# Kernel tuning notes

Hardware: AMD Instinct MI355X
Metric: run time of the kernel (lower is better)

## Reference

```python
import jax, jax.numpy as jnp
import numpy as np

TAU = 1.2  # relaxed-categorical temperature (forward default)


def setup_inputs() -> dict:
    key = jax.random.key(0)
    ks = jax.random.split(key, 8)
    B, F, V, E, H, T = 1024, 2048, 4096, 256, 1024, 32
    n = lambda k, shape: jax.random.normal(k, shape, jnp.float32) * 0.1
    return {
        "t": jax.random.normal(ks[0], (B, F), jnp.float32),
        "embedding": n(ks[1], (V, E)),
        "aff_w": n(ks[2], (H, F)),
        "aff_b": jnp.zeros((H,), jnp.float32),
        "w_ih": n(ks[3], (4 * H, E)),
        "w_hh": n(ks[4], (4 * H, H)),
        "b_ih": jnp.zeros((4 * H,), jnp.float32),
        # PyTorch init: forget-gate bias (second quarter) set to 1
        "b_hh": jnp.zeros((4 * H,), jnp.float32).at[H:2 * H].set(1.0),
        "lp_w": n(ks[5], (V, H)),
        "lp_b": jnp.zeros((V,), jnp.float32),
        "start_token_idx": 1,
        "max_sentence_length": T,
    }


def reference(t, embedding, aff_w, aff_b, w_ih, w_hh, b_ih, b_hh, lp_w, lp_b,
              start_token_idx, max_sentence_length):
    B = t.shape[0]
    H = aff_w.shape[0]
    V = embedding.shape[0]

    h0 = t @ aff_w.T + aff_b                      # [B, H]
    c0 = jnp.zeros((B, H), t.dtype)
    tok0 = jax.nn.one_hot(jnp.full((B,), start_token_idx), V, dtype=t.dtype)

    # Gumbel noise for RelaxedOneHotCategorical rsample, one slab per step
    gumbel = jax.random.gumbel(jax.random.key(42), (max_sentence_length, B, V), t.dtype)

    def step(carry, g):
        h, c, tok = carry
        emb = tok @ embedding                     # [B, E] (one-hot/relaxed matmul)
        gates = emb @ w_ih.T + b_ih + h @ w_hh.T + b_hh  # [B, 4H]
        i, f, gg, o = jnp.split(gates, 4, axis=-1)        # PyTorch gate order i,f,g,o
        c = jax.nn.sigmoid(f) * c + jax.nn.sigmoid(i) * jnp.tanh(gg)
        h = jax.nn.sigmoid(o) * jnp.tanh(c)
        # softmax probs -> relaxed sample: softmax((log p + G)/tau)
        logp = jax.nn.log_softmax(h @ lp_w.T + lp_b, axis=-1)  # [B, V]
        y = jax.nn.softmax((logp + g) / TAU, axis=-1)
        hard = jax.nn.one_hot(jnp.argmax(y, axis=-1), V, dtype=y.dtype)
        tok = jax.lax.stop_gradient(hard - y) + y  # straight-through
        return (h, c, tok), tok

    _, toks = jax.lax.scan(step, (h0, c0, tok0), gumbel)  # toks: [T, B, V]
    message = jnp.concatenate([tok0[None], toks], axis=0)  # [T+1, B, V]
    return jnp.transpose(message, (1, 0, 2))               # [B, T+1, V]
```

## Files before the change

kernel.cpp:

```cpp
#include <hip/hip_runtime.h>
#include <math.h>


typedef _Float16 f16;
typedef f16 f16x8 __attribute__((ext_vector_type(8)));
typedef float f32x4 __attribute__((ext_vector_type(4)));

#define F16_MIN_NORM 6.104e-5f

__device__ __forceinline__ void split_f16(float v, f16& h, f16& l) {
  f16 h0 = (fabsf(v) < F16_MIN_NORM) ? (f16)0.0f : (f16)v;
  float r = (v - (float)h0) * 4096.0f;
  h = h0; l = (f16)r;
}

__device__ __forceinline__ float sigm(float x) { return 1.0f / (1.0f + expf(-x)); }

#define GLOAD_LDS16(gsrc, ldst)                                               \
  __builtin_amdgcn_global_load_lds(                                           \
      (const __attribute__((address_space(1))) unsigned int*)(const void*)(gsrc), \
      (__attribute__((address_space(3))) unsigned int*)(void*)(ldst), 16, 0, 0)


__device__ __forceinline__ unsigned tf_rotl(unsigned x, int r) {
  return (x << r) | (x >> (32 - r));
}

__device__ inline float gumbel_at(unsigned idx) {
  const unsigned ks0 = 0u;
  const unsigned ks1 = 42u;
  const unsigned ks2 = 0x1BD11BDAu ^ ks0 ^ ks1;
  unsigned x0 = 0u + ks0;
  unsigned x1 = idx + ks1;
#define TFR(rot) { x0 += x1; x1 = tf_rotl(x1, rot); x1 ^= x0; }
  TFR(13) TFR(15) TFR(26) TFR(6)
  x0 += ks1; x1 += ks2 + 1u;
  TFR(17) TFR(29) TFR(16) TFR(24)
  x0 += ks2; x1 += ks0 + 2u;
  TFR(13) TFR(15) TFR(26) TFR(6)
  x0 += ks0; x1 += ks1 + 3u;
  TFR(17) TFR(29) TFR(16) TFR(24)
  x0 += ks1; x1 += ks2 + 4u;
  TFR(13) TFR(15) TFR(26) TFR(6)
  x0 += ks2; x1 += ks0 + 5u;
#undef TFR
  const unsigned bits = x0 ^ x1;
  const float f = __uint_as_float((bits >> 9) | 0x3F800000u) - 1.0f;
  const float tiny = 1.17549435082228751e-38f;
  const float u = fmaxf(tiny, f * (1.0f - tiny) + tiny);
  return -logf(-logf(u));
}


__global__ void init_kernel(float* __restrict__ out, const int* __restrict__ startp,
                            int* __restrict__ tok, int Tp1, int V) {
  const int b = blockIdx.x;
  const int start = *startp;
  if (threadIdx.x == 0) tok[b] = start;
  float* orow = out + (size_t)b * Tp1 * V;
  const int tq = start >> 2;
  for (int v4 = threadIdx.x; v4 < V / 4; v4 += blockDim.x) {
    float4 v = make_float4(0.f, 0.f, 0.f, 0.f);
    if (v4 == tq) ((float*)&v)[start & 3] = 1.0f;
    ((float4*)orow)[v4] = v;
  }
}

__global__ void pack_gates_kernel(const float* __restrict__ wih,
                                  const float* __restrict__ whh,
                                  f16* __restrict__ w0, f16* __restrict__ w1,
                                  int E, int H, int K) {
  const int k = blockIdx.x * blockDim.x + threadIdx.x;
  const int p = blockIdx.y;
  if (k >= K) return;
  const int n = ((p >> 4) & 3) * H + ((p >> 6) << 4) + (p & 15);
  const float v = (k < E) ? wih[(size_t)n * E + k] : whh[(size_t)n * H + (k - E)];
  f16 h, l; split_f16(v, h, l);
  w0[(size_t)p * K + k] = h;
  w1[(size_t)p * K + k] = l;
}

__global__ void pack_bias_kernel(const float* __restrict__ bih,
                                 const float* __restrict__ bhh,
                                 float* __restrict__ bi, float* __restrict__ bh, int H) {
  const int p = blockIdx.x * blockDim.x + threadIdx.x;
  const int n = ((p >> 4) & 3) * H + ((p >> 6) << 4) + (p & 15);
  bi[p] = bih[n];
  bh[p] = bhh[n];
}

__global__ void split_kernel(const float* __restrict__ in,
                             f16* __restrict__ o0, f16* __restrict__ o1, int n) {
  const int i = blockIdx.x * blockDim.x + threadIdx.x;
  if (i < n) { f16 h, l; split_f16(in[i], h, l); o0[i] = h; o1[i] = l; }
}


__device__ __forceinline__ void stage_chunk(
    int chunk, int srow, int scol,
    const f16* __restrict__ a0s, const f16* __restrict__ a1s, int lda, int ka, int bm,
    const f16* __restrict__ b0s, const f16* __restrict__ b1s, int ldb, int kb, int bn,
    f16 (*ldsA0)[32], f16 (*ldsA1)[32], f16 (*ldsB0)[32], f16 (*ldsB1)[32])
{
  if (chunk < 8) {
    GLOAD_LDS16(a0s + (size_t)(bm + chunk * 16 + srow) * lda + ka + scol,
                &ldsA0[chunk * 16][0]);
  } else if (chunk < 16) {
    const int s = chunk - 8;
    GLOAD_LDS16(a1s + (size_t)(bm + s * 16 + srow) * lda + ka + scol,
                &ldsA1[s * 16][0]);
  } else if (chunk < 24) {
    const int s = chunk - 16;
    GLOAD_LDS16(b0s + (size_t)(bn + s * 16 + srow) * ldb + kb + scol,
                &ldsB0[s * 16][0]);
  } else {
    const int s = chunk - 24;
    GLOAD_LDS16(b1s + (size_t)(bn + s * 16 + srow) * ldb + kb + scol,
                &ldsB1[s * 16][0]);
  }
}

#define MFMA_DECLS                                                            \
  const int tid  = threadIdx.x;                                               \
  const int lane = tid & 63;                                                  \
  const int wid  = tid >> 6;                                                  \
  const int bm   = blockIdx.y * 128;                                          \
  const int bn   = blockIdx.x * 128;                                          \
  const int wm   = (wid & 3) * 32;                                            \
  const int wn   = (wid >> 2) * 64;                                           \
  const int fr   = lane & 15;                                                 \
  const int fk   = (((lane >> 4) ^ ((lane >> 1) & 3)) * 8);                   \
  const int srow = lane >> 2;                                                 \
  const int scol = (((lane & 3) ^ ((lane >> 3) & 3)) * 8);                    \
  f32x4 acc0[2][4], acc1[2][4];                                               \
  _Pragma("unroll") for (int i = 0; i < 2; ++i)                               \
  _Pragma("unroll") for (int j = 0; j < 4; ++j) {                             \
    acc0[i][j] = (f32x4)0.0f; acc1[i][j] = (f32x4)0.0f; }

#define MFMA_LDS_DECL                                                         \
  __shared__ f16 ldsA0[4][128][32], ldsA1[4][128][32],                        \
                 ldsB0[4][128][32], ldsB1[4][128][32];

#define MFMA_STAGE_TO(buf, a0s, a1s, lda, ka, b0s, b1s, ldb, kb)              \
  { _Pragma("unroll") for (int c = 0; c < 4; ++c)                             \
      stage_chunk(wid * 4 + c, srow, scol, (a0s), (a1s), (lda), (ka), bm,     \
                  (b0s), (b1s), (ldb), (kb), bn,                              \
                  ldsA0[(buf)], ldsA1[(buf)], ldsB0[(buf)], ldsB1[(buf)]); }

#define MFMA_COMPUTE_FROM(buf)                                                \
  {                                                                           \
    f16x8 a0[2], a1[2], b0[4], b1[4];                                         \
    _Pragma("unroll") for (int i = 0; i < 2; ++i) {                           \
      a0[i] = *(const f16x8*)&ldsA0[(buf)][wm + i * 16 + fr][fk];             \
      a1[i] = *(const f16x8*)&ldsA1[(buf)][wm + i * 16 + fr][fk];             \
    }                                                                         \
    _Pragma("unroll") for (int j = 0; j < 4; ++j) {                           \
      b0[j] = *(const f16x8*)&ldsB0[(buf)][wn + j * 16 + fr][fk];             \
      b1[j] = *(const f16x8*)&ldsB1[(buf)][wn + j * 16 + fr][fk];             \
    }                                                                         \
    _Pragma("unroll") for (int i = 0; i < 2; ++i)                             \
    _Pragma("unroll") for (int j = 0; j < 4; ++j) {                           \
      acc0[i][j] = __builtin_amdgcn_mfma_f32_16x16x32_f16(a0[i], b0[j], acc0[i][j], 0, 0, 0); \
      acc1[i][j] = __builtin_amdgcn_mfma_f32_16x16x32_f16(a0[i], b1[j], acc1[i][j], 0, 0, 0); \
      acc1[i][j] = __builtin_amdgcn_mfma_f32_16x16x32_f16(a1[i], b0[j], acc1[i][j], 0, 0, 0); \
    }                                                                         \
  }

#define PIPE(NT)                                                              \
  STAGE_T(0, 0)                                                               \
  STAGE_T(1, 1)                                                               \
  STAGE_T(2, 2)                                                               \
  for (int t = 0; t < (NT); ++t) {                                            \
    asm volatile("" ::: "memory");                                            \
    if (t + 3 < (NT)) { STAGE_T(((t + 3) & 3), (t + 3)) }                     \
    const int rem = (NT) - 1 - t;                                             \
    if (rem >= 3)      asm volatile("s_waitcnt vmcnt(12)" ::: "memory");      \
    else if (rem == 2) asm volatile("s_waitcnt vmcnt(8)" ::: "memory");       \
    else if (rem == 1) asm volatile("s_waitcnt vmcnt(4)" ::: "memory");       \
    else               asm volatile("s_waitcnt vmcnt(0)" ::: "memory");       \
    __builtin_amdgcn_s_barrier();                                             \
    asm volatile("" ::: "memory");                                            \
    __builtin_amdgcn_s_setprio(1);                                            \
    MFMA_COMPUTE_FROM((t & 3))                                                \
    __builtin_amdgcn_s_setprio(0);                                            \
    asm volatile("" ::: "memory");                                            \
    __builtin_amdgcn_s_barrier();                                             \
  }

__global__ __launch_bounds__(512, 2) void h0_kernel(
    const f16* __restrict__ t0, const f16* __restrict__ t1, int F,
    const f16* __restrict__ aw0, const f16* __restrict__ aw1,
    const float* __restrict__ affb,
    f16* __restrict__ h0p, f16* __restrict__ h1p, int H,
    float* __restrict__ czero)
{
  MFMA_LDS_DECL
  MFMA_DECLS
  const int NT = F / 32;
#define STAGE_T(buf, t) MFMA_STAGE_TO(buf, t0, t1, F, (t) * 32, aw0, aw1, F, (t) * 32)
  PIPE(NT)
#undef STAGE_T
  const int q4 = (lane >> 4) * 4;
  const float s12 = 1.0f / 4096.0f;
  const int cn0 = bn + wn;
#pragma unroll
  for (int j = 0; j < 4; ++j) {
    const int col = cn0 + j * 16 + fr;
    const float bb = affb[col];
#pragma unroll
    for (int i = 0; i < 2; ++i) {
#pragma unroll
      for (int r = 0; r < 4; ++r) {
        const int row = bm + wm + i * 16 + q4 + r;
        const float v = (acc0[i][j][r] + acc1[i][j][r] * s12) + bb;
        f16 hh, hl; split_f16(v, hh, hl);
        const size_t off = (size_t)row * H + col;
        h0p[off] = hh; h1p[off] = hl;
        czero[off] = 0.0f;
      }
    }
  }
}

__global__ __launch_bounds__(512, 2) void gih_kernel(
    const f16* __restrict__ e0, const f16* __restrict__ e1, int E,
    const f16* __restrict__ w0, const f16* __restrict__ w1, int K,
    const float* __restrict__ bi, const float* __restrict__ bh,
    float* __restrict__ gih, int NP)
{
  MFMA_LDS_DECL
  MFMA_DECLS
  const int NT = E / 32;
#define STAGE_T(buf, t) MFMA_STAGE_TO(buf, e0, e1, E, (t) * 32, w0, w1, K, (t) * 32)
  PIPE(NT)
#undef STAGE_T
  const int q4 = (lane >> 4) * 4;
  const float s12 = 1.0f / 4096.0f;
  const int cn0 = bn + wn;
#pragma unroll
  for (int j = 0; j < 4; ++j) {
    const int col = cn0 + j * 16 + fr;
    const float bb = bi[col] + bh[col];
#pragma unroll
    for (int i = 0; i < 2; ++i)
#pragma unroll
      for (int r = 0; r < 4; ++r) {
        const int row = bm + wm + i * 16 + q4 + r;
        gih[(size_t)row * NP + col] = (acc0[i][j][r] + acc1[i][j][r] * s12) + bb;
      }
  }
}

__global__ __launch_bounds__(512, 2) void gates_kernel(
    const f16* __restrict__ hin0, const f16* __restrict__ hin1, int H,
    const f16* __restrict__ w0, const f16* __restrict__ w1, int K, int E,
    const float* __restrict__ gih, int NP, const int* __restrict__ tok,
    float* __restrict__ cbuf,
    f16* __restrict__ hout0, f16* __restrict__ hout1)
{
  MFMA_LDS_DECL
  MFMA_DECLS
  const int NT = H / 32;
#define STAGE_T(buf, t) MFMA_STAGE_TO(buf, hin0, hin1, H, (t) * 32, w0, w1, K, E + (t) * 32)
  PIPE(NT)
#undef STAGE_T
  const int q4 = (lane >> 4) * 4;
  const float s12 = 1.0f / 4096.0f;
  const int cn0 = bn + wn;
  const int nunit = (cn0 >> 2) + fr;
#pragma unroll
  for (int i = 0; i < 2; ++i) {
#pragma unroll
    for (int r = 0; r < 4; ++r) {
      const int row = bm + wm + i * 16 + q4 + r;
      const float* gr = gih + (size_t)tok[row] * NP + cn0 + fr;
      float gv[4];
#pragma unroll
      for (int j = 0; j < 4; ++j)
        gv[j] = (acc0[i][j][r] + acc1[i][j][r] * s12) + gr[j * 16];
      const size_t off = (size_t)row * H + nunit;
      const float c = cbuf[off];
      const float cn = __fadd_rn(__fmul_rn(sigm(gv[1]), c),
                                 __fmul_rn(sigm(gv[0]), tanhf(gv[2])));
      const float hn = __fmul_rn(sigm(gv[3]), tanhf(cn));
      cbuf[off] = cn;
      f16 hh, hl; split_f16(hn, hh, hl);
      hout0[off] = hh; hout1[off] = hl;
    }
  }
}

__global__ __launch_bounds__(512, 2) void logits_kernel(
    const f16* __restrict__ h0p, const f16* __restrict__ h1p, int H,
    const f16* __restrict__ w0, const f16* __restrict__ w1,
    const float* __restrict__ lpb,
    float* __restrict__ partM, int* __restrict__ partI,
    int step, int B, int V)
{
  MFMA_LDS_DECL
  MFMA_DECLS
  const int NT = H / 32;
#define STAGE_T(buf, t) MFMA_STAGE_TO(buf, h0p, h1p, H, (t) * 32, w0, w1, H, (t) * 32)
  PIPE(NT)
#undef STAGE_T
  const int q4 = (lane >> 4) * 4;
  const float s12 = 1.0f / 4096.0f;
  const int cn0 = bn + wn;
  float bv[4];
#pragma unroll
  for (int j = 0; j < 4; ++j) bv[j] = lpb[cn0 + j * 16 + fr];
#pragma unroll
  for (int i = 0; i < 2; ++i)
#pragma unroll
    for (int j = 0; j < 4; ++j) {
      const int col = cn0 + j * 16 + fr;
#pragma unroll
      for (int r = 0; r < 4; ++r) {
        const int row = bm + wm + i * 16 + q4 + r;
        const float logit = (acc0[i][j][r] + acc1[i][j][r] * s12) + bv[j];
        const unsigned gidx = ((unsigned)(step * B + row)) * (unsigned)V + (unsigned)col;
        acc0[i][j][r] = logit + gumbel_at(gidx);
      }
    }
  const int grp = cn0 >> 6;
#pragma unroll
  for (int i = 0; i < 2; ++i) {
#pragma unroll
    for (int r = 0; r < 4; ++r) {
      float mx = -INFINITY; int ix = 0;
#pragma unroll
      for (int j = 0; j < 4; ++j) {
        const float w = acc0[i][j][r];
        const int col = cn0 + j * 16 + fr;
        if (w > mx) { mx = w; ix = col; }
      }
#pragma unroll
      for (int m = 1; m < 16; m <<= 1) {
        const float om = __shfl_xor(mx, m, 64);
        const int oi = __shfl_xor(ix, m, 64);
        if (om > mx || (om == mx && oi < ix)) { mx = om; ix = oi; }
      }
      if (fr == 0) {
        const int row = bm + wm + i * 16 + q4 + r;
        partM[(size_t)row * 64 + grp] = mx;
        partI[(size_t)row * 64 + grp] = ix;
      }
    }
  }
}

__global__ __launch_bounds__(256) void finalize_kernel(
    const float* __restrict__ partM, const int* __restrict__ partI,
    float* __restrict__ out, int* __restrict__ tok,
    int step, int Tp1, int V)
{
  const int b = blockIdx.x;
  const int tid = threadIdx.x;
  __shared__ int s_tok;

  if (tid < 64) {
    float mx = partM[(size_t)b * 64 + tid];
    int ix = partI[(size_t)b * 64 + tid];
#pragma unroll
    for (int m = 1; m < 64; m <<= 1) {
      const float om = __shfl_xor(mx, m, 64);
      const int oi = __shfl_xor(ix, m, 64);
      if (om > mx || (om == mx && oi < ix)) { mx = om; ix = oi; }
    }
    if (tid == 0) { s_tok = ix; tok[b] = ix; }
  }
  __syncthreads();
  const int tk = s_tok;

  float* orow = out + ((size_t)b * Tp1 + step + 1) * V;
  const int tq = tk >> 2;
#pragma unroll
  for (int j = 0; j < 4; ++j) {
    const int idx = tid + 256 * j;
    float4 v = make_float4(0.f, 0.f, 0.f, 0.f);
    if (idx == tq) ((float*)&v)[tk & 3] = 1.0f;
    ((float4*)orow)[idx] = v;
  }
}


extern "C" void kernel_launch(void* const* d_in, const int* in_sizes, int n_in,
                              void* d_out, int out_size, void* d_ws, size_t ws_size,
                              hipStream_t stream) {
  const float* t     = (const float*)d_in[0];
  const float* emb   = (const float*)d_in[1];
  const float* affw  = (const float*)d_in[2];
  const float* affb  = (const float*)d_in[3];
  const float* wih   = (const float*)d_in[4];
  const float* whh   = (const float*)d_in[5];
  const float* bih   = (const float*)d_in[6];
  const float* bhh   = (const float*)d_in[7];
  const float* lpw   = (const float*)d_in[8];
  const float* lpb   = (const float*)d_in[9];
  const int*   start = (const int*)d_in[10];
  float* out = (float*)d_out;

  const int H = in_sizes[3];
  const int V = in_sizes[9];
  const int E = in_sizes[1] / V;
  const int F = in_sizes[2] / H;
  const int B = in_sizes[0] / F;
  const int Tp1 = out_size / (B * V);
  const int T = Tp1 - 1;
  const int KG = E + H;
  const int NP = 4 * H;

  char* p = (char*)d_ws;
  float* gihb  = (float*)p; p += (size_t)V * NP * 4;
  float* cbuf  = (float*)p; p += (size_t)B * H * 4;
  f16* hA0[2]; f16* hA1[2];
  hA0[0] = (f16*)p; p += (size_t)B * H * 2;
  hA1[0] = (f16*)p; p += (size_t)B * H * 2;
  hA0[1] = (f16*)p; p += (size_t)B * H * 2;
  hA1[1] = (f16*)p; p += (size_t)B * H * 2;
  f16* wg0 = (f16*)p; p += (size_t)V * KG * 2;
  f16* wg1 = (f16*)p; p += (size_t)V * KG * 2;
  f16* wl0 = (f16*)p; p += (size_t)V * H * 2;
  f16* wl1 = (f16*)p; p += (size_t)V * H * 2;
  f16* t0  = (f16*)p; p += (size_t)B * F * 2;
  f16* t1  = (f16*)p; p += (size_t)B * F * 2;
  f16* aw0 = (f16*)p; p += (size_t)H * F * 2;
  f16* aw1 = (f16*)p; p += (size_t)H * F * 2;
  f16* em0 = (f16*)p; p += (size_t)V * E * 2;
  f16* em1 = (f16*)p; p += (size_t)V * E * 2;
  float* bgi = (float*)p; p += (size_t)NP * 4;
  float* bgh = (float*)p; p += (size_t)NP * 4;
  float* partM = (float*)p; p += (size_t)B * 64 * 4;
  int*   partI = (int*)p;   p += (size_t)B * 64 * 4;
  int*   tokb  = (int*)p;   p += (size_t)B * 4;
  (void)ws_size; (void)n_in;

  init_kernel<<<B, 256, 0, stream>>>(out, start, tokb, Tp1, V);
  pack_gates_kernel<<<dim3((KG + 255) / 256, NP), 256, 0, stream>>>(
      wih, whh, wg0, wg1, E, H, KG);
  pack_bias_kernel<<<NP / 256, 256, 0, stream>>>(bih, bhh, bgi, bgh, H);
  split_kernel<<<(V * H + 255) / 256, 256, 0, stream>>>(lpw, wl0, wl1, V * H);
  split_kernel<<<(B * F + 255) / 256, 256, 0, stream>>>(t, t0, t1, B * F);
  split_kernel<<<(H * F + 255) / 256, 256, 0, stream>>>(affw, aw0, aw1, H * F);
  split_kernel<<<(V * E + 255) / 256, 256, 0, stream>>>(emb, em0, em1, V * E);
  h0_kernel<<<dim3(H / 128, B / 128), 512, 0, stream>>>(
      t0, t1, F, aw0, aw1, affb, hA0[0], hA1[0], H, cbuf);
  gih_kernel<<<dim3(NP / 128, V / 128), 512, 0, stream>>>(
      em0, em1, E, wg0, wg1, KG, bgi, bgh, gihb, NP);

  for (int s = 0; s < T; ++s) {
    const int cur = s & 1, nxt = (s + 1) & 1;
    gates_kernel<<<dim3(NP / 128, B / 128), 512, 0, stream>>>(
        hA0[cur], hA1[cur], H, wg0, wg1, KG, E, gihb, NP, tokb,
        cbuf, hA0[nxt], hA1[nxt]);
    logits_kernel<<<dim3(V / 128, B / 128), 512, 0, stream>>>(
        hA0[nxt], hA1[nxt], H, wl0, wl1, lpb,
        partM, partI, s, B, V);
    finalize_kernel<<<B, 256, 0, stream>>>(
        partM, partI, out, tokb, s, Tp1, V);
  }
}
```

Before: 3.954 ms.

## Unroll MFMA pipeline by four with one barrier per iteration

Reworks the 4-buffer LDS pipeline so each iteration waits for outstanding loads, takes a single barrier, issues the next stage's global->LDS load, then computes. The loop is unrolled four times so buffer indices are compile-time constants. This removes the trailing barrier per iteration and the runtime branching on the remaining tile count. The risk is that the single barrier must still stop the next stage from overwriting a buffer that other waves are still reading, and the epilogue assumes NT is a multiple of four.

After: 3.779 ms. -4.4%, faster.

```diff
diff --git a/kernel.cpp b/kernel.cpp
--- a/kernel.cpp
+++ b/kernel.cpp
@@ -166,25 +166,31 @@
     }                                                                         \
   }
 
+#define PIPE_ITER(buf, DOSTAGE, VM)                                           \
+  asm volatile("s_waitcnt vmcnt(" #VM ")" ::: "memory");                      \
+  __builtin_amdgcn_s_barrier();                                               \
+  asm volatile("" ::: "memory");                                              \
+  DOSTAGE                                                                     \
+  asm volatile("" ::: "memory");                                              \
+  __builtin_amdgcn_s_setprio(1);                                              \
+  MFMA_COMPUTE_FROM(buf)                                                      \
+  __builtin_amdgcn_s_setprio(0);                                              \
+  asm volatile("" ::: "memory");
+
 #define PIPE(NT)                                                              \
-  STAGE_T(0, 0)                                                               \
-  STAGE_T(1, 1)                                                               \
-  STAGE_T(2, 2)                                                               \
-  for (int t = 0; t < (NT); ++t) {                                            \
-    asm volatile("" ::: "memory");                                            \
-    if (t + 3 < (NT)) { STAGE_T(((t + 3) & 3), (t + 3)) }                     \
-    const int rem = (NT) - 1 - t;                                             \
-    if (rem >= 3)      asm volatile("s_waitcnt vmcnt(12)" ::: "memory");      \
-    else if (rem == 2) asm volatile("s_waitcnt vmcnt(8)" ::: "memory");       \
-    else if (rem == 1) asm volatile("s_waitcnt vmcnt(4)" ::: "memory");       \
-    else               asm volatile("s_waitcnt vmcnt(0)" ::: "memory");       \
-    __builtin_amdgcn_s_barrier();                                             \
-    asm volatile("" ::: "memory");                                            \
-    __builtin_amdgcn_s_setprio(1);                                            \
-    MFMA_COMPUTE_FROM((t & 3))                                                \
-    __builtin_amdgcn_s_setprio(0);                                            \
-    asm volatile("" ::: "memory");                                            \
-    __builtin_amdgcn_s_barrier();                                             \
+  STAGE_T(0, 0) STAGE_T(1, 1) STAGE_T(2, 2)                                   \
+  {                                                                           \
+    int tt = 0;                                                               \
+    for (; tt + 4 < (NT); tt += 4) {                                          \
+      PIPE_ITER(0, STAGE_T(3, tt + 3), 8)                                     \
+      PIPE_ITER(1, STAGE_T(0, tt + 4), 8)                                     \
+      PIPE_ITER(2, STAGE_T(1, tt + 5), 8)                                     \
+      PIPE_ITER(3, STAGE_T(2, tt + 6), 8)                                     \
+    }                                                                         \
+    PIPE_ITER(0, STAGE_T(3, tt + 3), 8)                                       \
+    PIPE_ITER(1, {}, 8)                                                       \
+    PIPE_ITER(2, {}, 4)                                                       \
+    PIPE_ITER(3, {}, 0)                                                       \
   }
 
 __global__ __launch_bounds__(512, 2) void h0_kernel(
```
